# Performance work log

Measured on AMD Instinct MI355X. Metric: run time of the kernel, lower is better.

The kernel has to match this reference:

```python
import jax, jax.numpy as jnp
import numpy as np

LOSS_WEIGHT = 1.0


def _norm_gram(feat):
    # feat: [B, C, H, W] -> normalized channel gram [B, C, C]
    B, C, H, W = feat.shape
    F = feat.reshape(B, C, H * W)                      # [B, C, HW]
    gram = jnp.einsum('bcn,bdn->bcd', F, F)            # [B, C, C]
    n = jnp.sqrt(jnp.sum(F * F, axis=2))               # [B, C] per-channel L2 norm
    norm_M = n[:, :, None] * n[:, None, :]             # [B, C, C]
    return gram / norm_M


def setup_inputs() -> dict:
    key = jax.random.key(0)
    k1, k2 = jax.random.split(key)
    det = jax.random.normal(k1, (8, 512, 128, 128), dtype=jnp.float32)
    sr = jax.random.normal(k2, (8, 512, 128, 128), dtype=jnp.float32)
    return {"det": det, "sr": sr}


def reference(det, sr):
    sm_det = _norm_gram(det)
    sm_sr = _norm_gram(sr)
    # use_l2=True -> MSELoss (mean reduction); weighted_loss with weight=None,
    # reduction='mean' on a scalar is identity; then * loss_weight.
    loss = jnp.mean((sm_det - sm_sr) ** 2)
    return loss * LOSS_WEIGHT
```

## Files before the change

kernel.cpp:

```cpp
#include <hip/hip_runtime.h>
#include <hip/hip_bf16.h>

#define C_CH 512
#define HW 16384
#define NB 8
#define TILE 128
#define BK 32
#define NTB 4
#define NTILES 10
#define KSPLIT 8
#define KCHUNK (HW / KSPLIT)
#define KSTEPS (KCHUNK / BK)
#define NGRAM 16
#define CC (C_CH * C_CH)
#define LOSS_BLOCKS 1024
#define GRID (NGRAM * KSPLIT * NTILES)
#define PANEL_SLOTS (TILE * 8)

typedef float f32x4 __attribute__((ext_vector_type(4)));
typedef __bf16 bf16x8 __attribute__((ext_vector_type(8)));

#define GLOAD_LDS16(gsrc, ldst)                                                 \
    __builtin_amdgcn_global_load_lds(                                           \
        (const __attribute__((address_space(1))) void*)(gsrc),                  \
        (__attribute__((address_space(3))) void*)(ldst), 16, 0, 0)

__global__ __launch_bounds__(256, 2) void gram_kernel(const float* __restrict__ det,
                                                      const float* __restrict__ sr,
                                                      float* __restrict__ gram) {
    const int bid = (int)blockIdx.x;
    const int lbid = (bid & 7) * (GRID / 8) + (bid >> 3);
    const int t = lbid % NTILES;
    const int gk = lbid / NTILES;
    const int ks = gk & (KSPLIT - 1);
    const int g = gk >> 3;
    const int tensor = g >> 3, b = g & 7;

    int ti = 0, tt = t;
    while (tt >= NTB - ti) { tt -= NTB - ti; ++ti; }
    const int tj = ti + tt;
    const bool diag = (ti == tj);

    const float* F = (tensor ? sr : det) + (size_t)b * C_CH * HW;
    const float* Abase = F + (size_t)(ti * TILE) * HW + ks * KCHUNK;
    const float* Bbase = F + (size_t)(tj * TILE) * HW + ks * KCHUNK;

    __shared__ f32x4 lds[2][2][PANEL_SLOTS];

    const int tid = threadIdx.x;
    const int lane = tid & 63;
    const int wid = tid >> 6;
    const int wr = wid >> 1, wc = wid & 1;
    const int kg = lane >> 4;
    const int l15 = lane & 15;

    auto STAGE = [&](int buf, int kt) {
        const float* sA = Abase + kt * BK;
        #pragma unroll
        for (int q = 0; q < 4; ++q) {
            int f = q * 256 + tid;
            int R = f >> 3, s = f & 7;
            int c = s ^ (R & 7);
            GLOAD_LDS16(sA + (size_t)R * HW + c * 4, &lds[buf][0][f]);
        }
        if (!diag) {
            const float* sB = Bbase + kt * BK;
            #pragma unroll
            for (int q = 0; q < 4; ++q) {
                int f = q * 256 + tid;
                int R = f >> 3, s = f & 7;
                int c = s ^ (R & 7);
                GLOAD_LDS16(sB + (size_t)R * HW + c * 4, &lds[buf][1][f]);
            }
        }
    };

    auto rdfrag = [&](const f32x4* P, int R) {
        f32x4 lo = P[R * 8 + ((2 * kg) ^ (R & 7))];
        f32x4 hi = P[R * 8 + ((2 * kg + 1) ^ (R & 7))];
        bf16x8 h;
        #pragma unroll
        for (int i = 0; i < 4; ++i) { h[i] = (__bf16)lo[i]; h[4 + i] = (__bf16)hi[i]; }
        return h;
    };

    f32x4 acc[4][4] = {};
    auto COMPUTE = [&](int buf) {
        const f32x4* As = &lds[buf][0][0];
        const f32x4* Bs = diag ? As : &lds[buf][1][0];
        bf16x8 af[4], bfr[4];
        #pragma unroll
        for (int m = 0; m < 4; ++m) af[m] = rdfrag(As, wr * 64 + m * 16 + l15);
        #pragma unroll
        for (int n = 0; n < 4; ++n) bfr[n] = rdfrag(Bs, wc * 64 + n * 16 + l15);
        #pragma unroll
        for (int m = 0; m < 4; ++m)
            #pragma unroll
            for (int n = 0; n < 4; ++n)
                if (!diag || (wc * 64 + n * 16 + 16 > wr * 64 + m * 16))
                    acc[m][n] = __builtin_amdgcn_mfma_f32_16x16x32_bf16(af[m], bfr[n], acc[m][n], 0, 0, 0);
    };

    STAGE(0, 0);
    #pragma unroll 1
    for (int kt = 0; kt < KSTEPS; ++kt) {
        if (kt + 1 < KSTEPS) {
            STAGE((kt + 1) & 1, kt + 1);
            if (diag) asm volatile("s_waitcnt vmcnt(4)" ::: "memory");
            else      asm volatile("s_waitcnt vmcnt(8)" ::: "memory");
        } else {
            asm volatile("s_waitcnt vmcnt(0)" ::: "memory");
        }
        __builtin_amdgcn_s_barrier();
        asm volatile("" ::: "memory");
        COMPUTE(kt & 1);
        asm volatile("s_waitcnt lgkmcnt(0)" ::: "memory");
        __builtin_amdgcn_s_barrier();
        asm volatile("" ::: "memory");
    }

    float* gout = gram + (size_t)g * CC;
    const int rb = ti * TILE + wr * 64 + (kg << 2);
    const int cb = tj * TILE + wc * 64 + l15;
    #pragma unroll
    for (int m = 0; m < 4; ++m)
        #pragma unroll
        for (int n = 0; n < 4; ++n) {
            if (diag && (wc * 64 + n * 16 + 16 <= wr * 64 + m * 16)) continue;
            #pragma unroll
            for (int j = 0; j < 4; ++j)
                atomicAdd(&gout[(size_t)(rb + m * 16 + j) * C_CH + cb + n * 16], acc[m][n][j]);
        }
}

__global__ void norm_kernel(const float* __restrict__ gram, float* __restrict__ invn) {
    const int g = blockIdx.x, c = threadIdx.x;
    float v = gram[(size_t)g * CC + (size_t)c * C_CH + c];
    invn[g * C_CH + c] = 1.0f / sqrtf(v);
}

__global__ __launch_bounds__(256) void loss_kernel(const float* __restrict__ gram,
                                                   const float* __restrict__ invn,
                                                   float* __restrict__ partials) {
    const int tid = threadIdx.x;
    float s = 0.f;
    for (int idx = blockIdx.x * 256 + tid; idx < NB * CC; idx += LOSS_BLOCKS * 256) {
        int b = idx >> 18;
        int c = (idx >> 9) & 511;
        int d = idx & 511;
        int cc = c, dd = d;
        if (dd < cc) { int tmp = cc; cc = dd; dd = tmp; }
        float gd = gram[(size_t)b * CC + (size_t)cc * C_CH + dd];
        float gs = gram[(size_t)(8 + b) * CC + (size_t)cc * C_CH + dd];
        float sd = gd * invn[b * C_CH + c] * invn[b * C_CH + d];
        float ss = gs * invn[(8 + b) * C_CH + c] * invn[(8 + b) * C_CH + d];
        float diff = sd - ss;
        s += diff * diff;
    }
    #pragma unroll
    for (int off = 32; off > 0; off >>= 1) s += __shfl_down(s, off, 64);
    __shared__ float red[4];
    if ((tid & 63) == 0) red[tid >> 6] = s;
    __syncthreads();
    if (tid == 0) partials[blockIdx.x] = red[0] + red[1] + red[2] + red[3];
}

__global__ void final_kernel(const float* __restrict__ partials, float* __restrict__ out) {
    const int tid = threadIdx.x;
    float s = 0.f;
    for (int i = tid; i < LOSS_BLOCKS; i += 256) s += partials[i];
    #pragma unroll
    for (int off = 32; off > 0; off >>= 1) s += __shfl_down(s, off, 64);
    __shared__ float red[4];
    if ((tid & 63) == 0) red[tid >> 6] = s;
    __syncthreads();
    if (tid == 0) out[0] = (red[0] + red[1] + red[2] + red[3]) * (1.0f / (float)(NB * (size_t)CC));
}

extern "C" void kernel_launch(void* const* d_in, const int* in_sizes, int n_in,
                              void* d_out, int out_size, void* d_ws, size_t ws_size,
                              hipStream_t stream) {
    const float* det = (const float*)d_in[0];
    const float* sr  = (const float*)d_in[1];
    float* gram     = (float*)d_ws;
    float* invn     = gram + (size_t)NGRAM * CC;
    float* partials = invn + NGRAM * C_CH;
    float* out      = (float*)d_out;

    hipMemsetAsync(gram, 0, (size_t)NGRAM * CC * sizeof(float), stream);
    gram_kernel<<<GRID, 256, 0, stream>>>(det, sr, gram);
    norm_kernel<<<NGRAM, C_CH, 0, stream>>>(gram, invn);
    loss_kernel<<<LOSS_BLOCKS, 256, 0, stream>>>(gram, invn, partials);
    final_kernel<<<1, 256, 0, stream>>>(partials, out);
}
```

Before: 270.2 us.

## Drop LDS double buffering in favor of single buffer with MFMA priority boost

Replaces the two-stage LDS pipeline with a single buffer per panel, so each k-step loads, waits for all loads to finish, then computes. This halves LDS use so more blocks can be resident (the launch bound's min-blocks hint is also removed), relying on occupancy rather than intra-block prefetch to hide memory latency. It also raises wave priority around the MFMA sequence. The risk is exposed global-load latency every step if occupancy does not rise enough.

```diff
diff --git a/kernel.cpp b/kernel.cpp
--- a/kernel.cpp
+++ b/kernel.cpp
@@ -25,11 +25,10 @@
         (const __attribute__((address_space(1))) void*)(gsrc),                  \
         (__attribute__((address_space(3))) void*)(ldst), 16, 0, 0)
 
-__global__ __launch_bounds__(256, 2) void gram_kernel(const float* __restrict__ det,
-                                                      const float* __restrict__ sr,
-                                                      float* __restrict__ gram) {
-    const int bid = (int)blockIdx.x;
-    const int lbid = (bid & 7) * (GRID / 8) + (bid >> 3);
+__global__ __launch_bounds__(256) void gram_kernel(const float* __restrict__ det,
+                                                   const float* __restrict__ sr,
+                                                   float* __restrict__ gram) {
+    const int lbid = ((int)blockIdx.x & 7) * (GRID / 8) + ((int)blockIdx.x >> 3);
     const int t = lbid % NTILES;
     const int gk = lbid / NTILES;
     const int ks = gk & (KSPLIT - 1);
@@ -45,7 +44,7 @@
     const float* Abase = F + (size_t)(ti * TILE) * HW + ks * KCHUNK;
     const float* Bbase = F + (size_t)(tj * TILE) * HW + ks * KCHUNK;
 
-    __shared__ f32x4 lds[2][2][PANEL_SLOTS];
+    __shared__ f32x4 lds[2][PANEL_SLOTS];
 
     const int tid = threadIdx.x;
     const int lane = tid & 63;
@@ -54,14 +53,14 @@
     const int kg = lane >> 4;
     const int l15 = lane & 15;
 
-    auto STAGE = [&](int buf, int kt) {
+    auto STAGE = [&](int kt) {
         const float* sA = Abase + kt * BK;
         #pragma unroll
         for (int q = 0; q < 4; ++q) {
             int f = q * 256 + tid;
             int R = f >> 3, s = f & 7;
             int c = s ^ (R & 7);
-            GLOAD_LDS16(sA + (size_t)R * HW + c * 4, &lds[buf][0][f]);
+            GLOAD_LDS16(sA + (size_t)R * HW + c * 4, &lds[0][f]);
         }
         if (!diag) {
             const float* sB = Bbase + kt * BK;
@@ -70,7 +69,7 @@
                 int f = q * 256 + tid;
                 int R = f >> 3, s = f & 7;
                 int c = s ^ (R & 7);
-                GLOAD_LDS16(sB + (size_t)R * HW + c * 4, &lds[buf][1][f]);
+                GLOAD_LDS16(sB + (size_t)R * HW + c * 4, &lds[1][f]);
             }
         }
     };
@@ -85,35 +84,31 @@
     };
 
     f32x4 acc[4][4] = {};
-    auto COMPUTE = [&](int buf) {
-        const f32x4* As = &lds[buf][0][0];
-        const f32x4* Bs = diag ? As : &lds[buf][1][0];
+    auto COMPUTE = [&]() {
+        const f32x4* As = &lds[0][0];
+        const f32x4* Bs = diag ? As : &lds[1][0];
         bf16x8 af[4], bfr[4];
         #pragma unroll
         for (int m = 0; m < 4; ++m) af[m] = rdfrag(As, wr * 64 + m * 16 + l15);
         #pragma unroll
         for (int n = 0; n < 4; ++n) bfr[n] = rdfrag(Bs, wc * 64 + n * 16 + l15);
+        __builtin_amdgcn_s_setprio(1);
         #pragma unroll
         for (int m = 0; m < 4; ++m)
             #pragma unroll
             for (int n = 0; n < 4; ++n)
                 if (!diag || (wc * 64 + n * 16 + 16 > wr * 64 + m * 16))
                     acc[m][n] = __builtin_amdgcn_mfma_f32_16x16x32_bf16(af[m], bfr[n], acc[m][n], 0, 0, 0);
+        __builtin_amdgcn_s_setprio(0);
     };
 
-    STAGE(0, 0);
     #pragma unroll 1
     for (int kt = 0; kt < KSTEPS; ++kt) {
-        if (kt + 1 < KSTEPS) {
-            STAGE((kt + 1) & 1, kt + 1);
-            if (diag) asm volatile("s_waitcnt vmcnt(4)" ::: "memory");
-            else      asm volatile("s_waitcnt vmcnt(8)" ::: "memory");
-        } else {
-            asm volatile("s_waitcnt vmcnt(0)" ::: "memory");
-        }
+        STAGE(kt);
+        asm volatile("s_waitcnt vmcnt(0)" ::: "memory");
         __builtin_amdgcn_s_barrier();
         asm volatile("" ::: "memory");
-        COMPUTE(kt & 1);
+        COMPUTE();
         asm volatile("s_waitcnt lgkmcnt(0)" ::: "memory");
         __builtin_amdgcn_s_barrier();
         asm volatile("" ::: "memory");
```

Result: slower. 397.7 us (+47.2%).
